# Kernel optimization log

Measured on AMD Instinct MI355X. Metric: run time of the kernel, lower is better.

The kernel has to match this reference:

```python
import jax, jax.numpy as jnp
import numpy as np


def setup_inputs() -> dict:
    key = jax.random.key(0)
    ks = jax.random.split(key, 8)
    B, IN, H, OUT = 8192, 1024, 2048, 1024
    SIGMA_MIN, SIGMA_MAX, PHASE = 0.9, 0.999, 2.0 * np.pi
    # recurrence decay params, initialized as in the torch module
    rng = np.random.RandomState(0)
    u1 = rng.random_sample(H)
    u2 = rng.random_sample(H)
    v = -0.5 * np.log(u1 * (SIGMA_MAX ** 2 - SIGMA_MIN ** 2) + SIGMA_MIN ** 2)
    theta = u2 * PHASE
    scale_b = 1.0 / np.sqrt(IN)
    scale_c = 1.0 / np.sqrt(H)
    return {
        "x": jax.random.normal(ks[0], (B, IN), dtype=jnp.float32),
        "h_prev": jax.random.normal(ks[1], (B, H), dtype=jnp.float32),
        "Br": jax.random.normal(ks[2], (H, IN), dtype=jnp.float32) * scale_b,
        "Bi": jax.random.normal(ks[3], (H, IN), dtype=jnp.float32) * scale_b,
        "Cr": jax.random.normal(ks[4], (OUT, H), dtype=jnp.float32) * scale_c,
        "Ci": jax.random.normal(ks[5], (OUT, H), dtype=jnp.float32) * scale_c,
        "v_log": jnp.asarray(np.log(v), dtype=jnp.float32),
        "theta_log": jnp.asarray(np.log(theta), dtype=jnp.float32),
    }


def reference(x, h_prev, Br, Bi, Cr, Ci, v_log, theta_log):
    # effective diagonal recurrence weight w = exp(-exp(v_log) + i*exp(theta_log))
    mag = jnp.exp(-jnp.exp(v_log))            # [H]
    ang = jnp.exp(theta_log)                  # [H]
    wr = mag * jnp.cos(ang)
    wi = mag * jnp.sin(ang)
    # h = B(x) + h_prev * w  (h_prev is real -> imag part comes only from wi)
    # complexLinear on real x: real = x@Br^T, imag = x@Bi^T
    hr = jnp.einsum('bi,hi->bh', x, Br) + h_prev * wr   # [B,H]
    hi = jnp.einsum('bi,hi->bh', x, Bi) + h_prev * wi   # [B,H]
    # out = Re(C(h)) = hr@Cr^T - hi@Ci^T
    out = jnp.einsum('bh,oh->bo', hr, Cr) - jnp.einsum('bh,oh->bo', hi, Ci)
    return out
```

## Files before the change

kernel.cpp:

```cpp
#include <hip/hip_runtime.h>
#include <stdint.h>

typedef unsigned short u16;
typedef short bf16x8 __attribute__((ext_vector_type(8)));
typedef float f32x4 __attribute__((ext_vector_type(4)));

typedef void as1_void __attribute__((address_space(1)));
typedef void as3_void __attribute__((address_space(3)));

__device__ inline u16 f32_to_bf16(float f) {
    uint32_t u = __builtin_bit_cast(uint32_t, f);
    u += 0x7fffu + ((u >> 16) & 1u);
    return (u16)(u >> 16);
}

__device__ inline void gld_lds16(const void* g, void* l) {
    __builtin_amdgcn_global_load_lds((as1_void*)g, (as3_void*)l, 16, 0, 0);
}



__global__ void bigcast_kernel(const float* __restrict__ x,
                               const float* __restrict__ h_prev,
                               const float* __restrict__ Br,
                               const float* __restrict__ Bi,
                               u16* __restrict__ xh_bf,
                               u16* __restrict__ Bcat) {
    const int n4x = 8192 * 1024 / 4;
    const int tid = threadIdx.x;
    if (blockIdx.x < 24576) {
        int i = blockIdx.x * 256 + tid;
        float4 f = (i < n4x) ? ((const float4*)x)[i] : ((const float4*)h_prev)[i - n4x];
        ushort4 o;
        o.x = f32_to_bf16(f.x); o.y = f32_to_bf16(f.y);
        o.z = f32_to_bf16(f.z); o.w = f32_to_bf16(f.w);
        ((ushort4*)xh_bf)[i] = o;
    } else {
        __shared__ float t[32][33];
        int id2 = blockIdx.x - 24576;
        const float* src = (id2 >= 2048) ? Bi : Br;
        int colOff = (id2 >= 2048) ? 2048 : 0;
        int rem = id2 & 2047;
        int c0 = (rem & 31) * 32, r0 = (rem >> 5) * 32;
        int tx = tid & 31, ty = tid >> 5;
#pragma unroll
        for (int j = 0; j < 4; j++)
            t[ty + j * 8][tx] = src[(size_t)(r0 + ty + j * 8) * 1024 + c0 + tx];
        __syncthreads();
#pragma unroll
        for (int j = 0; j < 4; j++)
            Bcat[(size_t)(c0 + ty + j * 8) * 4096 + colOff + r0 + tx] =
                f32_to_bf16(t[tx][ty + j * 8]);
    }
}


__global__ void reduce_cw_kernel(const float* __restrict__ partials,
                                 const float* __restrict__ Cr, const float* __restrict__ Ci,
                                 const float* __restrict__ v_log, const float* __restrict__ th_log,
                                 u16* __restrict__ Wmain, u16* __restrict__ Cwbf) {
    const int n4_red = 1024 * 1024 / 4;
    const int n4_cw  = 1024 * 2048 / 4;
    int i = blockIdx.x * blockDim.x + threadIdx.x;
    if (i < n4_red) {
        int e = i * 4;
        float4 s = *(const float4*)(partials + e);
#pragma unroll
        for (int z = 1; z < 8; z++) {
            float4 p = *(const float4*)(partials + ((size_t)z << 20) + e);
            s.x += p.x; s.y += p.y; s.z += p.z; s.w += p.w;
        }
        ushort4 u;
        u.x = f32_to_bf16(s.x); u.y = f32_to_bf16(s.y);
        u.z = f32_to_bf16(s.z); u.w = f32_to_bf16(s.w);
        ((ushort4*)Wmain)[i] = u;
    } else if (i < n4_red + n4_cw) {
        int j = i - n4_red;
        int e = j * 4;
        int o = e >> 11;
        int h = e & 2047;
        float4 cr = *(const float4*)(Cr + (size_t)o * 2048 + h);
        float4 ci = *(const float4*)(Ci + (size_t)o * 2048 + h);
        float4 vl = *(const float4*)(v_log + h);
        float4 tl = *(const float4*)(th_log + h);
        float mag, ang;
        ushort4 u;
        mag = expf(-expf(vl.x)); ang = expf(tl.x);
        u.x = f32_to_bf16(cr.x * (mag * cosf(ang)) - ci.x * (mag * sinf(ang)));
        mag = expf(-expf(vl.y)); ang = expf(tl.y);
        u.y = f32_to_bf16(cr.y * (mag * cosf(ang)) - ci.y * (mag * sinf(ang)));
        mag = expf(-expf(vl.z)); ang = expf(tl.z);
        u.z = f32_to_bf16(cr.z * (mag * cosf(ang)) - ci.z * (mag * sinf(ang)));
        mag = expf(-expf(vl.w)); ang = expf(tl.w);
        u.w = f32_to_bf16(cr.w * (mag * cosf(ang)) - ci.w * (mag * sinf(ang)));
        ((ushort4*)Cwbf)[j] = u;
    }
}


__global__ __launch_bounds__(256)
void gemm_splitk_kernel(const float* __restrict__ Cr, const float* __restrict__ Ci,
                        const u16* __restrict__ Bcat, float* __restrict__ partials)
{
    __shared__ __align__(16) u16 ldsA[128 * 64];
    __shared__ __align__(16) u16 ldsB[128 * 64];

    const int tid = threadIdx.x, wid = tid >> 6, lane = tid & 63;
    const int quad = lane >> 4, l16 = lane & 15;
    const int wm = wid >> 1, wn = wid & 1;
    const int bm = blockIdx.y, bn = blockIdx.x, bz = blockIdx.z;

    const float* Asrc = (bz < 4) ? Cr : Ci;
    const uint32_t sgn_mask = (bz < 4) ? 0u : 0x80000000u;
    const int akb = (bz < 4) ? bz * 512 : bz * 512 - 2048;

    const int ar = tid >> 1;
    const int ac = (tid & 1) * 32;
    const float* agp = Asrc + (size_t)(bm * 128 + ar) * 2048 + akb + ac;

    const u16* gB[4];
    u16* lB[4];
#pragma unroll
    for (int t = 0; t < 4; t++) {
        int s = wid * 256 + t * 64 + lane;
        int sr = s >> 3;
        int sj = (s & 7) ^ (sr & 7);
        lB[t] = ldsB + s * 8;
        gB[t] = Bcat + (size_t)(bn * 128 + sr) * 4096 + sj * 8 + bz * 512;
    }

    const f32x4 fz = {0.f, 0.f, 0.f, 0.f};
    f32x4 acc[4][4];
#pragma unroll
    for (int i = 0; i < 4; i++)
#pragma unroll
        for (int j = 0; j < 4; j++) acc[i][j] = fz;

    for (int k0 = 0; k0 < 512; k0 += 64) {
        __syncthreads();
#pragma unroll
        for (int t = 0; t < 4; t++)
            gld_lds16(gB[t] + k0, lB[t]);
        float4 av[8];
#pragma unroll
        for (int q = 0; q < 8; q++)
            av[q] = *(const float4*)(agp + k0 + q * 4);
#pragma unroll
        for (int c = 0; c < 4; c++) {
            bf16x8 w;
            const float4 a0 = av[2 * c], a1 = av[2 * c + 1];
            w[0] = (short)f32_to_bf16(__builtin_bit_cast(float, __builtin_bit_cast(uint32_t, a0.x) ^ sgn_mask));
            w[1] = (short)f32_to_bf16(__builtin_bit_cast(float, __builtin_bit_cast(uint32_t, a0.y) ^ sgn_mask));
            w[2] = (short)f32_to_bf16(__builtin_bit_cast(float, __builtin_bit_cast(uint32_t, a0.z) ^ sgn_mask));
            w[3] = (short)f32_to_bf16(__builtin_bit_cast(float, __builtin_bit_cast(uint32_t, a0.w) ^ sgn_mask));
            w[4] = (short)f32_to_bf16(__builtin_bit_cast(float, __builtin_bit_cast(uint32_t, a1.x) ^ sgn_mask));
            w[5] = (short)f32_to_bf16(__builtin_bit_cast(float, __builtin_bit_cast(uint32_t, a1.y) ^ sgn_mask));
            w[6] = (short)f32_to_bf16(__builtin_bit_cast(float, __builtin_bit_cast(uint32_t, a1.z) ^ sgn_mask));
            w[7] = (short)f32_to_bf16(__builtin_bit_cast(float, __builtin_bit_cast(uint32_t, a1.w) ^ sgn_mask));
            int jg = (ac >> 3) + c;
            *(bf16x8*)(ldsA + (ar * 8 + (jg ^ (ar & 7))) * 8) = w;
        }
        __syncthreads();
#pragma unroll
        for (int ks = 0; ks < 2; ks++) {
            bf16x8 af[4], bfr[4];
#pragma unroll
            for (int i = 0; i < 4; i++) {
                int r = wm * 64 + i * 16 + l16;
                af[i] = *(const bf16x8*)(ldsA + (r * 8 + ((ks * 4 + quad) ^ (r & 7))) * 8);
            }
#pragma unroll
            for (int j = 0; j < 4; j++) {
                int r = wn * 64 + j * 16 + l16;
                bfr[j] = *(const bf16x8*)(ldsB + (r * 8 + ((ks * 4 + quad) ^ (r & 7))) * 8);
            }
#pragma unroll
            for (int i = 0; i < 4; i++)
#pragma unroll
                for (int j = 0; j < 4; j++)
                    acc[i][j] = __builtin_amdgcn_mfma_f32_16x16x32_bf16(af[i], bfr[j], acc[i][j], 0, 0, 0);
        }
    }

    float* P = partials + ((size_t)bz << 20);
    const int gm = bm * 128 + wm * 64, gn = bn * 128 + wn * 64;
#pragma unroll
    for (int i = 0; i < 4; i++)
#pragma unroll
        for (int j = 0; j < 4; j++) {
            int col = gn + j * 16 + l16;
#pragma unroll
            for (int r = 0; r < 4; r++)
                P[(size_t)(gm + i * 16 + quad * 4 + r) * 1024 + col] = acc[i][j][r];
        }
}


__global__ __launch_bounds__(256)
void gemm_main_kernel(const u16* __restrict__ Axb, const u16* __restrict__ Ahb,
                      const u16* __restrict__ Bw,  const u16* __restrict__ Bcw,
                      float* __restrict__ out)
{
    __shared__ __align__(16) u16 ldsA[128 * 64];
    __shared__ __align__(16) u16 ldsB[128 * 64];

    const int tid = threadIdx.x, wid = tid >> 6, lane = tid & 63;
    const int quad = lane >> 4, l16 = lane & 15;
    const int wm = wid >> 1, wn = wid & 1;
    const int id = blockIdx.x;
    const int bm = id & 63, bn = id >> 6;

    int srow[4], sj[4];
    u16 *lA[4], *lB[4];
#pragma unroll
    for (int t = 0; t < 4; t++) {
        int s = wid * 256 + t * 64 + lane;
        srow[t] = s >> 3;
        sj[t] = (s & 7) ^ (srow[t] & 7);
        lA[t] = ldsA + s * 8;
        lB[t] = ldsB + s * 8;
    }

    const f32x4 fz = {0.f, 0.f, 0.f, 0.f};
    f32x4 acc[4][4];
#pragma unroll
    for (int i = 0; i < 4; i++)
#pragma unroll
        for (int j = 0; j < 4; j++) acc[i][j] = fz;

#pragma unroll 1
    for (int phase = 0; phase < 2; phase++) {
        const u16* Ap = phase ? Ahb : Axb;
        const u16* Bp = phase ? Bcw : Bw;
        const int KS = phase ? 2048 : 1024;
        const u16* gA[4]; const u16* gB[4];
#pragma unroll
        for (int t = 0; t < 4; t++) {
            gA[t] = Ap + (size_t)(bm * 128 + srow[t]) * KS + sj[t] * 8;
            gB[t] = Bp + (size_t)(bn * 128 + srow[t]) * KS + sj[t] * 8;
        }
        for (int k0 = 0; k0 < KS; k0 += 64) {
            __syncthreads();
#pragma unroll
            for (int t = 0; t < 4; t++) {
                gld_lds16(gA[t] + k0, lA[t]);
                gld_lds16(gB[t] + k0, lB[t]);
            }
            __syncthreads();
#pragma unroll
            for (int ks = 0; ks < 2; ks++) {
                bf16x8 af[4], bfr[4];
#pragma unroll
                for (int i = 0; i < 4; i++) {
                    int r = wm * 64 + i * 16 + l16;
                    af[i] = *(const bf16x8*)(ldsA + (r * 8 + ((ks * 4 + quad) ^ (r & 7))) * 8);
                }
#pragma unroll
                for (int j = 0; j < 4; j++) {
                    int r = wn * 64 + j * 16 + l16;
                    bfr[j] = *(const bf16x8*)(ldsB + (r * 8 + ((ks * 4 + quad) ^ (r & 7))) * 8);
                }
#pragma unroll
                for (int i = 0; i < 4; i++)
#pragma unroll
                    for (int j = 0; j < 4; j++)
                        acc[i][j] = __builtin_amdgcn_mfma_f32_16x16x32_bf16(af[i], bfr[j], acc[i][j], 0, 0, 0);
            }
        }
    }

    const int gm = bm * 128 + wm * 64, gn = bn * 128 + wn * 64;
#pragma unroll
    for (int i = 0; i < 4; i++)
#pragma unroll
        for (int j = 0; j < 4; j++) {
            int col = gn + j * 16 + l16;
#pragma unroll
            for (int r = 0; r < 4; r++)
                out[(size_t)(gm + i * 16 + quad * 4 + r) * 1024 + col] = acc[i][j][r];
        }
}


extern "C" void kernel_launch(void* const* d_in, const int* in_sizes, int n_in,
                              void* d_out, int out_size, void* d_ws, size_t ws_size,
                              hipStream_t stream)
{
    const float* x      = (const float*)d_in[0];
    const float* h_prev = (const float*)d_in[1];
    const float* Br     = (const float*)d_in[2];
    const float* Bi     = (const float*)d_in[3];
    const float* Cr     = (const float*)d_in[4];
    const float* Ci     = (const float*)d_in[5];
    const float* v_log  = (const float*)d_in[6];
    const float* th_log = (const float*)d_in[7];
    float* out = (float*)d_out;

    const size_t MB = 1024 * 1024;
    size_t need = 94 * MB;
    if (ws_size < need) return;

    char* ws = (char*)d_ws;
    u16*   xh_bf    = (u16*)ws;
    u16*   x_bf     = xh_bf;
    u16*   hp_bf    = (u16*)(ws + 16 * MB);
    u16*   Bcat     = (u16*)(ws + 48 * MB);
    float* partials = (float*)(ws + 56 * MB);
    u16*   Wmain    = (u16*)(ws + 88 * MB);
    u16*   Cwbf     = (u16*)(ws + 90 * MB);

    bigcast_kernel<<<28672, 256, 0, stream>>>(x, h_prev, Br, Bi, xh_bf, Bcat);
    gemm_splitk_kernel<<<dim3(8, 8, 8), 256, 0, stream>>>(Cr, Ci, Bcat, partials);
    reduce_cw_kernel<<<3072, 256, 0, stream>>>(partials, Cr, Ci, v_log, th_log, Wmain, Cwbf);
    gemm_main_kernel<<<512, 256, 0, stream>>>(x_bf, hp_bf, Wmain, Cwbf, out);
}
```

Measured before the change: 258.8 us.

## Overlap split-K weight GEMM with activation casts in one prep kernel

Moves the x/h_prev bf16 cast and the Cw computation into the same launch as the split-K weight-product GEMM, so the 256 GEMM blocks run alongside the bandwidth-bound cast blocks instead of in separate sequential launches. Split-K depth is halved from 8 to 4 slices of 1024, which reduces the partial buffer and the reduction traffic. The Br/Bi transpose-cast becomes its own small kernel. The trade-off is fewer GEMM blocks with longer K loops, and these heavy blocks may end up as a tail if the scheduler dispatches them alongside the cast blocks.

```diff
diff --git a/kernel.cpp b/kernel.cpp
--- a/kernel.cpp
+++ b/kernel.cpp
@@ -20,99 +20,80 @@
 
 
 
-__global__ void bigcast_kernel(const float* __restrict__ x,
-                               const float* __restrict__ h_prev,
-                               const float* __restrict__ Br,
-                               const float* __restrict__ Bi,
-                               u16* __restrict__ xh_bf,
-                               u16* __restrict__ Bcat) {
-    const int n4x = 8192 * 1024 / 4;
+__global__ void transpose_cast_kernel(const float* __restrict__ Br,
+                                      const float* __restrict__ Bi,
+                                      u16* __restrict__ Bcat) {
+    __shared__ float t[32][33];
+    const float* src = blockIdx.z ? Bi : Br;
+    int colOff = blockIdx.z ? 2048 : 0;
+    int c0 = blockIdx.x * 32, r0 = blockIdx.y * 32;
+    int tx = threadIdx.x, ty = threadIdx.y;
+#pragma unroll
+    for (int j = 0; j < 4; j++)
+        t[ty + j * 8][tx] = src[(size_t)(r0 + ty + j * 8) * 1024 + c0 + tx];
+    __syncthreads();
+#pragma unroll
+    for (int j = 0; j < 4; j++)
+        Bcat[(size_t)(c0 + ty + j * 8) * 4096 + colOff + r0 + tx] =
+            f32_to_bf16(t[tx][ty + j * 8]);
+}
+
+
+__global__ __launch_bounds__(256)
+void megaprep_kernel(const float* __restrict__ Cr, const float* __restrict__ Ci,
+                     const u16* __restrict__ Bcat, float* __restrict__ partials,
+                     const float* __restrict__ x, const float* __restrict__ h_prev,
+                     u16* __restrict__ xh_bf,
+                     const float* __restrict__ v_log, const float* __restrict__ th_log,
+                     u16* __restrict__ Cwbf)
+{
     const int tid = threadIdx.x;
-    if (blockIdx.x < 24576) {
-        int i = blockIdx.x * 256 + tid;
-        float4 f = (i < n4x) ? ((const float4*)x)[i] : ((const float4*)h_prev)[i - n4x];
-        ushort4 o;
-        o.x = f32_to_bf16(f.x); o.y = f32_to_bf16(f.y);
-        o.z = f32_to_bf16(f.z); o.w = f32_to_bf16(f.w);
-        ((ushort4*)xh_bf)[i] = o;
-    } else {
-        __shared__ float t[32][33];
-        int id2 = blockIdx.x - 24576;
-        const float* src = (id2 >= 2048) ? Bi : Br;
-        int colOff = (id2 >= 2048) ? 2048 : 0;
-        int rem = id2 & 2047;
-        int c0 = (rem & 31) * 32, r0 = (rem >> 5) * 32;
-        int tx = tid & 31, ty = tid >> 5;
-#pragma unroll
-        for (int j = 0; j < 4; j++)
-            t[ty + j * 8][tx] = src[(size_t)(r0 + ty + j * 8) * 1024 + c0 + tx];
-        __syncthreads();
-#pragma unroll
-        for (int j = 0; j < 4; j++)
-            Bcat[(size_t)(c0 + ty + j * 8) * 4096 + colOff + r0 + tx] =
-                f32_to_bf16(t[tx][ty + j * 8]);
-    }
-}
-
-
-__global__ void reduce_cw_kernel(const float* __restrict__ partials,
-                                 const float* __restrict__ Cr, const float* __restrict__ Ci,
-                                 const float* __restrict__ v_log, const float* __restrict__ th_log,
-                                 u16* __restrict__ Wmain, u16* __restrict__ Cwbf) {
-    const int n4_red = 1024 * 1024 / 4;
-    const int n4_cw  = 1024 * 2048 / 4;
-    int i = blockIdx.x * blockDim.x + threadIdx.x;
-    if (i < n4_red) {
-        int e = i * 4;
-        float4 s = *(const float4*)(partials + e);
-#pragma unroll
-        for (int z = 1; z < 8; z++) {
-            float4 p = *(const float4*)(partials + ((size_t)z << 20) + e);
-            s.x += p.x; s.y += p.y; s.z += p.z; s.w += p.w;
-        }
-        ushort4 u;
-        u.x = f32_to_bf16(s.x); u.y = f32_to_bf16(s.y);
-        u.z = f32_to_bf16(s.z); u.w = f32_to_bf16(s.w);
-        ((ushort4*)Wmain)[i] = u;
-    } else if (i < n4_red + n4_cw) {
-        int j = i - n4_red;
-        int e = j * 4;
-        int o = e >> 11;
-        int h = e & 2047;
-        float4 cr = *(const float4*)(Cr + (size_t)o * 2048 + h);
-        float4 ci = *(const float4*)(Ci + (size_t)o * 2048 + h);
-        float4 vl = *(const float4*)(v_log + h);
-        float4 tl = *(const float4*)(th_log + h);
-        float mag, ang;
-        ushort4 u;
-        mag = expf(-expf(vl.x)); ang = expf(tl.x);
-        u.x = f32_to_bf16(cr.x * (mag * cosf(ang)) - ci.x * (mag * sinf(ang)));
-        mag = expf(-expf(vl.y)); ang = expf(tl.y);
-        u.y = f32_to_bf16(cr.y * (mag * cosf(ang)) - ci.y * (mag * sinf(ang)));
-        mag = expf(-expf(vl.z)); ang = expf(tl.z);
-        u.z = f32_to_bf16(cr.z * (mag * cosf(ang)) - ci.z * (mag * sinf(ang)));
-        mag = expf(-expf(vl.w)); ang = expf(tl.w);
-        u.w = f32_to_bf16(cr.w * (mag * cosf(ang)) - ci.w * (mag * sinf(ang)));
-        ((ushort4*)Cwbf)[j] = u;
-    }
-}
-
-
-__global__ __launch_bounds__(256)
-void gemm_splitk_kernel(const float* __restrict__ Cr, const float* __restrict__ Ci,
-                        const u16* __restrict__ Bcat, float* __restrict__ partials)
-{
+    const int blk = blockIdx.x;
+
+    if (blk >= 256) {
+        if (blk < 24832) {
+            const int n4x = 8192 * 1024 / 4;
+            int i = (blk - 256) * 256 + tid;
+            float4 f = (i < n4x) ? ((const float4*)x)[i] : ((const float4*)h_prev)[i - n4x];
+            ushort4 o;
+            o.x = f32_to_bf16(f.x); o.y = f32_to_bf16(f.y);
+            o.z = f32_to_bf16(f.z); o.w = f32_to_bf16(f.w);
+            ((ushort4*)xh_bf)[i] = o;
+        } else {
+            int j = (blk - 24832) * 256 + tid;
+            int e = j * 4;
+            int o = e >> 11;
+            int h = e & 2047;
+            float4 cr = *(const float4*)(Cr + (size_t)o * 2048 + h);
+            float4 ci = *(const float4*)(Ci + (size_t)o * 2048 + h);
+            float4 vl = *(const float4*)(v_log + h);
+            float4 tl = *(const float4*)(th_log + h);
+            float mag, ang;
+            ushort4 u;
+            mag = expf(-expf(vl.x)); ang = expf(tl.x);
+            u.x = f32_to_bf16(cr.x * (mag * cosf(ang)) - ci.x * (mag * sinf(ang)));
+            mag = expf(-expf(vl.y)); ang = expf(tl.y);
+            u.y = f32_to_bf16(cr.y * (mag * cosf(ang)) - ci.y * (mag * sinf(ang)));
+            mag = expf(-expf(vl.z)); ang = expf(tl.z);
+            u.z = f32_to_bf16(cr.z * (mag * cosf(ang)) - ci.z * (mag * sinf(ang)));
+            mag = expf(-expf(vl.w)); ang = expf(tl.w);
+            u.w = f32_to_bf16(cr.w * (mag * cosf(ang)) - ci.w * (mag * sinf(ang)));
+            ((ushort4*)Cwbf)[j] = u;
+        }
+        return;
+    }
+
     __shared__ __align__(16) u16 ldsA[128 * 64];
     __shared__ __align__(16) u16 ldsB[128 * 64];
 
-    const int tid = threadIdx.x, wid = tid >> 6, lane = tid & 63;
+    const int wid = tid >> 6, lane = tid & 63;
     const int quad = lane >> 4, l16 = lane & 15;
     const int wm = wid >> 1, wn = wid & 1;
-    const int bm = blockIdx.y, bn = blockIdx.x, bz = blockIdx.z;
-
-    const float* Asrc = (bz < 4) ? Cr : Ci;
-    const uint32_t sgn_mask = (bz < 4) ? 0u : 0x80000000u;
-    const int akb = (bz < 4) ? bz * 512 : bz * 512 - 2048;
+    const int bn = blk & 7, bm = (blk >> 3) & 7, bz = blk >> 6;
+
+    const float* Asrc = (bz < 2) ? Cr : Ci;
+    const uint32_t sgn_mask = (bz < 2) ? 0u : 0x80000000u;
+    const int akb = (bz & 1) * 1024;
 
     const int ar = tid >> 1;
     const int ac = (tid & 1) * 32;
@@ -126,7 +107,7 @@
         int sr = s >> 3;
         int sj = (s & 7) ^ (sr & 7);
         lB[t] = ldsB + s * 8;
-        gB[t] = Bcat + (size_t)(bn * 128 + sr) * 4096 + sj * 8 + bz * 512;
+        gB[t] = Bcat + (size_t)(bn * 128 + sr) * 4096 + sj * 8 + bz * 1024;
     }
 
     const f32x4 fz = {0.f, 0.f, 0.f, 0.f};
@@ -136,7 +117,7 @@
 #pragma unroll
         for (int j = 0; j < 4; j++) acc[i][j] = fz;
 
-    for (int k0 = 0; k0 < 512; k0 += 64) {
+    for (int k0 = 0; k0 < 1024; k0 += 64) {
         __syncthreads();
 #pragma unroll
         for (int t = 0; t < 4; t++)
@@ -196,6 +177,23 @@
 }
 
 
+__global__ void reduce_w_kernel(const float* __restrict__ partials,
+                                u16* __restrict__ Wmain) {
+    int i = blockIdx.x * blockDim.x + threadIdx.x;
+    int e = i * 4;
+    float4 s = *(const float4*)(partials + e);
+#pragma unroll
+    for (int z = 1; z < 4; z++) {
+        float4 p = *(const float4*)(partials + ((size_t)z << 20) + e);
+        s.x += p.x; s.y += p.y; s.z += p.z; s.w += p.w;
+    }
+    ushort4 u;
+    u.x = f32_to_bf16(s.x); u.y = f32_to_bf16(s.y);
+    u.z = f32_to_bf16(s.z); u.w = f32_to_bf16(s.w);
+    ((ushort4*)Wmain)[i] = u;
+}
+
+
 __global__ __launch_bounds__(256)
 void gemm_main_kernel(const u16* __restrict__ Axb, const u16* __restrict__ Ahb,
                       const u16* __restrict__ Bw,  const u16* __restrict__ Bcw,
@@ -297,20 +295,20 @@
     float* out = (float*)d_out;
 
     const size_t MB = 1024 * 1024;
-    size_t need = 94 * MB;
+    size_t need = 78 * MB;
     if (ws_size < need) return;
 
     char* ws = (char*)d_ws;
-    u16*   xh_bf    = (u16*)ws;
-    u16*   x_bf     = xh_bf;
+    u16*   x_bf     = (u16*)ws;
     u16*   hp_bf    = (u16*)(ws + 16 * MB);
     u16*   Bcat     = (u16*)(ws + 48 * MB);
     float* partials = (float*)(ws + 56 * MB);
-    u16*   Wmain    = (u16*)(ws + 88 * MB);
-    u16*   Cwbf     = (u16*)(ws + 90 * MB);
-
-    bigcast_kernel<<<28672, 256, 0, stream>>>(x, h_prev, Br, Bi, xh_bf, Bcat);
-    gemm_splitk_kernel<<<dim3(8, 8, 8), 256, 0, stream>>>(Cr, Ci, Bcat, partials);
-    reduce_cw_kernel<<<3072, 256, 0, stream>>>(partials, Cr, Ci, v_log, th_log, Wmain, Cwbf);
+    u16*   Wmain    = (u16*)(ws + 72 * MB);
+    u16*   Cwbf     = (u16*)(ws + 74 * MB);
+
+    transpose_cast_kernel<<<dim3(32, 64, 2), dim3(32, 8), 0, stream>>>(Br, Bi, Bcat);
+    megaprep_kernel<<<26880, 256, 0, stream>>>(Cr, Ci, Bcat, partials,
+                                               x, h_prev, x_bf, v_log, th_log, Cwbf);
+    reduce_w_kernel<<<1024, 256, 0, stream>>>(partials, Wmain);
     gemm_main_kernel<<<512, 256, 0, stream>>>(x_bf, hp_bf, Wmain, Cwbf, out);
 }
```

Measured after the change: 273.7 us. 1.06x slower.
